# Kernel tuning notes

Hardware: AMD Instinct MI355X
Metric: run time of the kernel (lower is better)

## Reference

```python
import jax, jax.numpy as jnp
import numpy as np

B, L, H, NH, HD, IT = 16, 512, 256, 8, 32, 2
NEG = -9e15


def _ln(x, g, b):
    m = x.mean(-1, keepdims=True)
    v = ((x - m) ** 2).mean(-1, keepdims=True)
    return (x - m) / jnp.sqrt(v + 1e-5) * g + b


def setup_inputs() -> dict:
    key = jax.random.key(0)
    ks = jax.random.split(key, 12)

    def nrm(k, shape, fan_in):
        return jax.random.normal(k, shape, dtype=jnp.float32) / np.float32(np.sqrt(fan_in))

    return {
        "data": jax.random.normal(ks[0], (B, L, H), jnp.float32),
        "gat_WQ_w": nrm(ks[1], (NH, H, H), H),
        "gat_WQ_b": jnp.zeros((NH, H), jnp.float32),
        "gat_a1": nrm(ks[2], (NH, 3 * H), 3 * H),
        "gat_a2": nrm(ks[3], (NH, 3 * H), 3 * H),
        "gat_fc_w": nrm(ks[4], (NH, 3 * H, HD), 3 * H),
        "gat_fc_b": jnp.zeros((NH, HD), jnp.float32),
        "norm_g": jnp.ones((IT, H), jnp.float32),
        "norm_b": jnp.zeros((IT, H), jnp.float32),
        "sq_w": nrm(ks[5], (IT, NH * HD, H), H),
        "sq_b": jnp.zeros((IT, NH * HD), jnp.float32),
        "sk_w": nrm(ks[6], (IT, NH * HD, H), H),
        "sk_b": jnp.zeros((IT, NH * HD), jnp.float32),
        "so_w": nrm(ks[7], (IT, H, NH * HD), NH * HD),
        "so_b": jnp.zeros((IT, H), jnp.float32),
        "fc_w": nrm(ks[8], (NH * HD, H), NH * HD),
        "fc_b": jnp.zeros((H,), jnp.float32),
        "mask": jax.random.randint(ks[9], (B, L), 0, 2, jnp.int32),
        "edge_matrix": jax.random.randint(ks[10], (B, L, L), 0, 2, jnp.int32),
    }


def _gat_head(xn, ax, adj_pos, Wq, bq, a1, a2, Fw, Fb):
    # xn: [B,L,H] normalized nodes; ax: [B,L,2H] interleaved (r_embs, relay)
    h = jnp.concatenate([xn @ Wq.T + bq, ax], axis=-1)  # [B,L,3H]
    # decomposed a^T [h_i ; h_j] = a1.h_i + a2.h_j  (avoids O(N^2*6H) concat)
    ei = h @ a1  # [B,L]
    ej = h @ a2  # [B,L]
    e = jax.nn.leaky_relu(ei[:, :, None] + ej[:, None, :], 0.2)  # [B,L,L]
    att = jax.nn.softmax(jnp.where(adj_pos, e, NEG), axis=2)
    hp = jnp.einsum('bij,bjd->bid', att, h)  # [B,L,3H]
    return jax.nn.elu(hp @ Fw + Fb)  # [B,L,HD]


def _forward(data, gat_WQ_w, gat_WQ_b, gat_a1, gat_a2, gat_fc_w, gat_fc_b,
             norm_g, norm_b, sq_w, sq_b, sk_w, sk_b, so_w, so_b, fc_w, fc_b,
             mask, edge_matrix):
    pad = mask == 0                                   # True at padding positions
    smask = jnp.concatenate([jnp.zeros((B, 1), bool), pad], axis=1)  # [B,L+1]
    adj_pos = edge_matrix > 0
    nodes = data                                      # [B,L,H]
    relay = data.mean(axis=1)                         # [B,H]
    gat = jax.vmap(_gat_head, in_axes=(None, None, None, 0, 0, 0, 0, 0, 0))
    scale = np.float32(1.0 / np.sqrt(HD))

    for i in range(IT):
        xn = _ln(nodes, norm_g[i], norm_b[i])
        # torch views [B,H,2,L] as [B,2H,L]: features interleave (r_embs, relay)
        ax = jnp.stack([data, jnp.broadcast_to(relay[:, None, :], (B, L, H))],
                       axis=-1).reshape(B, L, 2 * H)
        heads = gat(xn, ax, adj_pos, gat_WQ_w, gat_WQ_b, gat_a1, gat_a2,
                    gat_fc_w, gat_fc_b)               # [NH,B,L,HD]
        temp = jnp.transpose(heads, (1, 2, 0, 3)).reshape(B, L, NH * HD)
        nodes = nodes + jax.nn.leaky_relu(temp @ fc_w + fc_b, 0.01)
        # star attention (MSA2); note original uses v = k (WV unused)
        y = jnp.concatenate([relay[:, None, :], nodes], axis=1)   # [B,L+1,H]
        q = (relay @ sq_w[i].T + sq_b[i]).reshape(B, NH, HD)
        k = (y @ sk_w[i].T + sk_b[i]).transpose(0, 2, 1).reshape(B, NH, HD, L + 1)
        v = jnp.swapaxes(k, 2, 3)                                  # [B,NH,L+1,HD]
        pre = jnp.einsum('bnd,bndl->bnl', q, k) * scale
        pre = jnp.where(smask[:, None, :], -jnp.inf, pre)
        al = jax.nn.softmax(pre, axis=2)
        att = jnp.einsum('bnl,bnld->bnd', al, v).reshape(B, NH * HD)
        relay = jax.nn.leaky_relu(att @ so_w[i].T + so_b[i], 0.01)
        nodes = jnp.where(pad[:, :, None], 0.0, nodes)
    return nodes, relay


def reference(data, gat_WQ_w, gat_WQ_b, gat_a1, gat_a2, gat_fc_w, gat_fc_b,
              norm_g, norm_b, sq_w, sq_b, sk_w, sk_b, so_w, so_b, fc_w, fc_b,
              mask, edge_matrix):
    return _forward(data, gat_WQ_w, gat_WQ_b, gat_a1, gat_a2, gat_fc_w, gat_fc_b,
                    norm_g, norm_b, sq_w, sq_b, sk_w, sk_b, so_w, so_b, fc_w, fc_b,
                    mask, edge_matrix)
```

## Files before the change

### kernel.cpp

```cpp
#include <hip/hip_runtime.h>
#include <hip/hip_bf16.h>
#include <math.h>

#define BB 16
#define LL 512
#define HH 256
#define NHEAD 8
#define HDIM 32
#define LP1 513
#define NODES_ELEMS (BB*LL*HH)

typedef __attribute__((ext_vector_type(8))) short bf16x8;
typedef __attribute__((ext_vector_type(4))) float f32x4;

__device__ __forceinline__ unsigned short f2bf(float f) {
  union { float f; unsigned u; } x; x.f = f;
  unsigned r = x.u + 0x7fffu + ((x.u >> 16) & 1u);
  return (unsigned short)(r >> 16);
}
__device__ __forceinline__ float bf2f(unsigned short u) {
  union { unsigned u; float f; } x; x.u = (unsigned)u << 16; return x.f;
}

__global__ __launch_bounds__(256) void mega_prep_kernel(
    const float* __restrict__ data, const int* __restrict__ edge,
    const float* __restrict__ fc_w, const float* __restrict__ fcw,
    const float* __restrict__ sk_w, const float* __restrict__ sq_w,
    const float* __restrict__ so_w, const float* __restrict__ WQw,
    const float* __restrict__ WQb, const float* __restrict__ a1,
    const float* __restrict__ a2,
    unsigned short* __restrict__ datab, unsigned char* __restrict__ ep,
    unsigned short* __restrict__ fcwT, unsigned short* __restrict__ Bcat,
    unsigned short* __restrict__ skwb, float* __restrict__ sqT,
    float* __restrict__ soT, float* __restrict__ rpart,
    float* __restrict__ w1, float* __restrict__ w2,
    float* __restrict__ c1, float* __restrict__ c2,
    float* __restrict__ bqf, float* __restrict__ a1o, float* __restrict__ a2o) {
  __shared__ float smem[64 * 65];
  int blk = blockIdx.x, t = threadIdx.x;
  if (blk < 128) {
    int b = blk >> 3, ch = blk & 7;
    const float* pr = data + ((size_t)b * 512 + ch * 64) * 256 + t;
    unsigned short* db = datab + ((size_t)b * 512 + ch * 64) * 256 + t;
    float s = 0.f;
    for (int l = 0; l < 64; l++) {
      float v = pr[(size_t)l * 256];
      db[(size_t)l * 256] = f2bf(v);
      s += v;
    }
    rpart[(size_t)blk * 256 + t] = s;
  } else if (blk < 2176) {
    int row = (blk - 128) * 4 + (t >> 6);
    int lane = t & 63;
    const int* adj = edge + ((size_t)row << 9);
    unsigned v = 0;
#pragma unroll
    for (int u = 0; u < 8; u++) v |= (adj[lane + 64 * u] > 0 ? 1u : 0u) << u;
    ep[((size_t)row << 6) + lane] = (unsigned char)v;
  } else if (blk < 2432) {
    int idx = (blk - 2176) * 256 + t;
    int d = idx & 31;
    int g = idx >> 5;
    int n = g >> 8, c = g & 255;
    Bcat[((size_t)n * 32 + d) * 512 + 256 + c] =
        f2bf(fcw[((size_t)n * 768 + 256 + 2 * c) * 32 + d]);
  } else if (blk < 2944) {
    int idx = (blk - 2432) * 256 + t;
    skwb[idx] = f2bf(sk_w[idx]);
  } else if (blk < 3024) {
    int q = blk - 2944;
    int mat = q >> 4, tl = q & 15;
    int r0 = (tl >> 2) * 64, c0 = (tl & 3) * 64;
    const float* in;
    if (mat == 0) in = fc_w;
    else if (mat <= 2) in = sq_w + (mat - 1) * 65536;
    else in = so_w + (mat - 3) * 65536;
    int cc = t & 63, rq = t >> 6;
#pragma unroll
    for (int i = 0; i < 16; i++) {
      int r = rq + i * 4;
      smem[r * 65 + cc] = in[(r0 + r) * 256 + c0 + cc];
    }
    __syncthreads();
#pragma unroll
    for (int i = 0; i < 16; i++) {
      int cp = rq + i * 4;
      float v = smem[cc * 65 + cp];
      if (mat == 0) fcwT[(c0 + cp) * 256 + r0 + cc] = f2bf(v);
      else if (mat <= 2) sqT[(mat - 1) * 65536 + (c0 + cp) * 256 + r0 + cc] = v;
      else soT[(mat - 3) * 65536 + (c0 + cp) * 256 + r0 + cc] = v;
    }
  } else if (blk < 3152) {
    int q = blk - 3024;
    int n = q >> 4, kc = q & 15;
    int k = kc * 16 + (t & 15), cseg = t >> 4;
    float s1 = 0.f, s2 = 0.f;
#pragma unroll
    for (int u = 0; u < 16; u++) {
      int c = cseg * 16 + u;
      float wv = WQw[((size_t)(n * 256 + c)) * 256 + k];
      s1 = fmaf(a1[n * 768 + c], wv, s1);
      s2 = fmaf(a2[n * 768 + c], wv, s2);
    }
    smem[cseg * 16 + (t & 15)] = s1;
    smem[256 + cseg * 16 + (t & 15)] = s2;
    __syncthreads();
    if (cseg == 0) {
      float a = 0.f, b2 = 0.f;
#pragma unroll
      for (int u = 0; u < 16; u++) {
        a += smem[u * 16 + (t & 15)];
        b2 += smem[256 + u * 16 + (t & 15)];
      }
      w1[n * 256 + k] = a;
      w2[n * 256 + k] = b2;
    }
  } else if (blk < 3160) {
    int n = blk - 3152;
    int d = t & 31, seg = t >> 5;
    float s = 0.f;
#pragma unroll
    for (int u = 0; u < 32; u++) {
      int c = seg * 32 + u;
      s = fmaf(WQb[n * 256 + c], fcw[((size_t)n * 768 + c) * 32 + d], s);
    }
    smem[seg * 32 + d] = s;
    __syncthreads();
    if (seg == 0) {
      float a = 0.f;
#pragma unroll
      for (int u = 0; u < 8; u++) a += smem[u * 32 + d];
      bqf[n * 32 + d] = a;
    }
  } else if (blk == 3160) {
    int n = t >> 5, sl = t & 31;
    float s1 = 0.f, s2 = 0.f;
#pragma unroll
    for (int u = 0; u < 8; u++) {
      int c = sl * 8 + u;
      float wb = WQb[n * 256 + c];
      s1 = fmaf(a1[n * 768 + c], wb, s1);
      s2 = fmaf(a2[n * 768 + c], wb, s2);
    }
    smem[t] = s1; smem[256 + t] = s2;
    __syncthreads();
    if (sl == 0) {
      float a = 0.f, b2 = 0.f;
      for (int u = 0; u < 32; u++) { a += smem[n * 32 + u]; b2 += smem[256 + n * 32 + u]; }
      c1[n] = a; c2[n] = b2;
    }
  } else {
#pragma unroll
    for (int n = 0; n < 8; n++) {
      a1o[n * 256 + t] = a1[n * 768 + 256 + 2 * t];
      a2o[n * 256 + t] = a2[n * 768 + 256 + 2 * t];
    }
  }
}

__device__ __forceinline__ void rarf_tail(
    int n, int b, int t, const float* rel,
    const float* __restrict__ a1, const float* __restrict__ a2,
    const float* __restrict__ fcw, const float* __restrict__ fcb,
    const float* __restrict__ bqf,
    float* __restrict__ ra1, float* __restrict__ ra2, float* __restrict__ rf,
    float* red1, float* red2, float* pf_s) {
  int lane = t & 63, w = t >> 6;
  float p1 = rel[t] * a1[n * 768 + 257 + 2 * t];
  float p2 = rel[t] * a2[n * 768 + 257 + 2 * t];
#pragma unroll
  for (int o = 32; o; o >>= 1) { p1 += __shfl_xor(p1, o); p2 += __shfl_xor(p2, o); }
  if (lane == 0) { red1[w] = p1; red2[w] = p2; }
  int d = t & 31, seg = t >> 5;
  float pf = 0.f;
  for (int u = 0; u < 32; u++) {
    int k = seg * 32 + u;
    pf = fmaf(rel[k], fcw[((size_t)n * 768 + 257 + 2 * k) * 32 + d], pf);
  }
  pf_s[seg * 33 + d] = pf;
  __syncthreads();
  if (t == 0) {
    ra1[n * 16 + b] = red1[0] + red1[1] + red1[2] + red1[3];
    ra2[n * 16 + b] = red2[0] + red2[1] + red2[2] + red2[3];
  }
  if (t < 32) {
    float s = 0.f;
    for (int gg = 0; gg < 8; gg++) s += pf_s[gg * 33 + t];
    rf[((size_t)n * 16 + b) * 32 + t] = s + fcb[n * 32 + t] + bqf[n * 32 + t];
  }
}

__global__ __launch_bounds__(256) void prep2_kernel(
    const float* __restrict__ WQw, const float* __restrict__ fcw,
    unsigned short* __restrict__ Bcat,
    const float* __restrict__ rpart,
    const unsigned short* __restrict__ skw0, const float* __restrict__ skb0,
    const float* __restrict__ a1, const float* __restrict__ a2,
    const float* __restrict__ fcb, const float* __restrict__ bqf,
    const float* __restrict__ w1, const float* __restrict__ w2,
    const float* __restrict__ a1o, const float* __restrict__ a2o,
    float* __restrict__ relay, unsigned short* __restrict__ ktb,
    float* __restrict__ ra1, float* __restrict__ ra2, float* __restrict__ rf) {
  __shared__ float smem[12288];
  int blk = blockIdx.x, t = threadIdx.x;
  if (blk < 128) {
    float* wq_s = smem;
    float* fw_s = smem + 4096;
    int n = blk >> 4, kt = blk & 15;
#pragma unroll
    for (int i = 0; i < 16; i++) {
      int c = i * 16 + (t >> 4), kk = t & 15;
      wq_s[c * 16 + kk] = WQw[(size_t)n * 65536 + c * 256 + kt * 16 + kk];
    }
#pragma unroll
    for (int i = 0; i < 32; i++) {
      int idx = i * 256 + t;
      fw_s[(idx >> 5) * 32 + (idx & 31)] = fcw[(size_t)n * 24576 + idx];
    }
    __syncthreads();
    int kloc = t >> 4, dp = t & 15;
    float a0 = 0.f, a1v = 0.f;
    for (int c = 0; c < 256; c++) {
      float wv = wq_s[c * 16 + kloc];
      a0 = fmaf(wv, fw_s[c * 32 + dp * 2], a0);
      a1v = fmaf(wv, fw_s[c * 32 + dp * 2 + 1], a1v);
    }
    int k = kt * 16 + kloc;
    Bcat[((size_t)n * 32 + dp * 2) * 512 + k] = f2bf(a0);
    Bcat[((size_t)n * 32 + dp * 2 + 1) * 512 + k] = f2bf(a1v);
  } else if (blk < 256) {
    float* rel = smem;
    float* red1 = smem + 256;
    float* red2 = smem + 264;
    float* pf_s = smem + 272;
    int id = blk - 128;
    int n = id >> 4, b = id & 15;
    float s = 0.f;
#pragma unroll
    for (int ch = 0; ch < 8; ch++) s += rpart[((size_t)(b * 8 + ch)) * 256 + t];
    s *= (1.0f / 512.0f);
    rel[t] = s;
    __syncthreads();
    if (n == 0) {
      relay[b * 256 + t] = s;
      float acc = 0.f;
      for (int k = 0; k < 256; k++) acc = fmaf(rel[k], bf2f(skw0[(size_t)t * 256 + k]), acc);
      ktb[((size_t)b * LP1) * 256 + t] = f2bf(acc + skb0[t]);
    }
    rarf_tail(n, b, t, rel, a1, a2, fcw, fcb, bqf, ra1, ra2, rf, red1, red2, pf_s);
  } else {
    int q = blk - 256;
    int n = q & 7, isEj = q >> 3;
    const float* wsrc = isEj ? w2 : w1;
    const float* asrc = isEj ? a2o : a1o;
#pragma unroll
    for (int h = 0; h < 2; h++) {
      int k = h * 256 + t;
      float v = (k < 256) ? wsrc[n * 256 + k] : asrc[n * 256 + k - 256];
      Bcat[((size_t)(256 + q)) * 512 + k] = f2bf(v);
    }
  }
}

__global__ __launch_bounds__(256) void so_rarf_kernel(
    const float* __restrict__ atts,
    const float* __restrict__ soT_it, const float* __restrict__ sob_it,
    const unsigned short* __restrict__ skw_nx, const float* __restrict__ skb_nx,
    const float* __restrict__ a1, const float* __restrict__ a2,
    const float* __restrict__ fcw, const float* __restrict__ fcb,
    const float* __restrict__ bqf, int do_extras,
    float* __restrict__ relay, unsigned short* __restrict__ ktb,
    float* __restrict__ ra1, float* __restrict__ ra2, float* __restrict__ rf) {
  int n = blockIdx.x >> 4, b = blockIdx.x & 15;
  if (!do_extras && n > 0) return;
  __shared__ float xr[256];
  __shared__ float rel[256];
  __shared__ float red1[4], red2[4];
  __shared__ float pf_s[8 * 33];
  int t = threadIdx.x;
  xr[t] = atts[b * 256 + t];
  __syncthreads();
  float acc = 0.f;
  for (int k = 0; k < 256; k++) acc = fmaf(xr[k], soT_it[(size_t)k * 256 + t], acc);
  float v = acc + sob_it[t];
  v = v > 0.f ? v : 0.01f * v;
  rel[t] = v;
  __syncthreads();
  if (n == 0) relay[b * 256 + t] = v;
  if (!do_extras) return;
  if (n == 0) {
    float a2v = 0.f;
    for (int k = 0; k < 256; k++) a2v = fmaf(rel[k], bf2f(skw_nx[(size_t)t * 256 + k]), a2v);
    ktb[((size_t)b * LP1) * 256 + t] = f2bf(a2v + skb_nx[t]);
  }
  rarf_tail(n, b, t, rel, a1, a2, fcw, fcb, bqf, ra1, ra2, rf, red1, red2, pf_s);
}

__global__ __launch_bounds__(256) void lng_gemm_kernel(
    const float* __restrict__ src,
    const unsigned short* __restrict__ datab,
    const unsigned short* __restrict__ Bcat,
    const float* __restrict__ g, const float* __restrict__ bb,
    const float* __restrict__ c1, const float* __restrict__ c2,
    const float* __restrict__ ra1, const float* __restrict__ ra2,
    unsigned short* __restrict__ GT,
    float* __restrict__ ei, float* __restrict__ ej) {
  __shared__ unsigned short A[32][520];
  int blk = blockIdx.x;
  int b = blk >> 4;
  int i0 = (blk & 15) << 5;
  int t = threadIdx.x;
  int wv = t >> 6, lane = t & 63;
  int lo = lane & 15, quad = lane >> 4;

  float4 g4 = *(const float4*)(g + lane * 4);
  float4 b4 = *(const float4*)(bb + lane * 4);
  float xs[8][4];
  float sum[8], sq[8];
#pragma unroll
  for (int rr = 0; rr < 8; rr++) {
    int grow = b * 512 + i0 + wv * 8 + rr;
    float4 v = *(const float4*)(src + (size_t)grow * 256 + lane * 4);
    xs[rr][0] = v.x; xs[rr][1] = v.y; xs[rr][2] = v.z; xs[rr][3] = v.w;
    sum[rr] = v.x + v.y + v.z + v.w;
    sq[rr] = v.x * v.x + v.y * v.y + v.z * v.z + v.w * v.w;
    ushort4 dv4 = *(const ushort4*)(datab + (size_t)grow * 256 + lane * 4);
    *(ushort4*)&A[wv * 8 + rr][256 + lane * 4] = dv4;
  }
#pragma unroll
  for (int o = 32; o; o >>= 1) {
#pragma unroll
    for (int rr = 0; rr < 8; rr++) {
      sum[rr] += __shfl_xor(sum[rr], o);
      sq[rr] += __shfl_xor(sq[rr], o);
    }
  }
#pragma unroll
  for (int rr = 0; rr < 8; rr++) {
    float mean = sum[rr] * (1.0f / 256.0f);
    float var = sq[rr] * (1.0f / 256.0f) - mean * mean;
    float rstd = rsqrtf(var + 1e-5f);
    ushort4 pk;
    pk.x = f2bf((xs[rr][0] - mean) * rstd * g4.x + b4.x);
    pk.y = f2bf((xs[rr][1] - mean) * rstd * g4.y + b4.y);
    pk.z = f2bf((xs[rr][2] - mean) * rstd * g4.z + b4.z);
    pk.w = f2bf((xs[rr][3] - mean) * rstd * g4.w + b4.w);
    *(ushort4*)&A[wv * 8 + rr][lane * 4] = pk;
  }
  __syncthreads();

  f32x4 acc[2][4] = {};
  f32x4 acce[2] = {};
  for (int k0 = 0; k0 < 512; k0 += 32) {
    bf16x8 af[2];
#pragma unroll
    for (int rt = 0; rt < 2; rt++)
      af[rt] = *(const bf16x8*)&A[rt * 16 + lo][k0 + quad * 8];
#pragma unroll
    for (int j = 0; j < 4; j++) {
      int tile = j * 4 + wv;
      bf16x8 bf_ = *(const bf16x8*)(Bcat + (size_t)(tile * 16 + lo) * 512 + k0 + quad * 8);
#pragma unroll
      for (int rt = 0; rt < 2; rt++)
        acc[rt][j] = __builtin_amdgcn_mfma_f32_16x16x32_bf16(af[rt], bf_, acc[rt][j], 0, 0, 0);
    }
    if (wv == 0) {
      bf16x8 bf_ = *(const bf16x8*)(Bcat + (size_t)(256 + lo) * 512 + k0 + quad * 8);
#pragma unroll
      for (int rt = 0; rt < 2; rt++)
        acce[rt] = __builtin_amdgcn_mfma_f32_16x16x32_bf16(af[rt], bf_, acce[rt], 0, 0, 0);
    }
  }
#pragma unroll
  for (int j = 0; j < 4; j++) {
    int tile = j * 4 + wv;
    int co = tile * 16 + lo;
    int n = co >> 5, d = co & 31;
#pragma unroll
    for (int rt = 0; rt < 2; rt++) {
      int jj = i0 + rt * 16 + quad * 4;
      ushort4 pk;
      pk.x = f2bf(acc[rt][j][0]);
      pk.y = f2bf(acc[rt][j][1]);
      pk.z = f2bf(acc[rt][j][2]);
      pk.w = f2bf(acc[rt][j][3]);
      *(ushort4*)&GT[(((size_t)(n * 16 + b) * 32 + d) << 9) + jj] = pk;
    }
  }
  if (wv == 0) {
    int n = lo & 7, isEj = lo >> 3;
    float cst = isEj ? (c2[n] + ra2[n * 16 + b]) : (c1[n] + ra1[n * 16 + b]);
    float* outp = isEj ? ej : ei;
#pragma unroll
    for (int rt = 0; rt < 2; rt++) {
#pragma unroll
      for (int r = 0; r < 4; r++) {
        int row = i0 + rt * 16 + quad * 4 + r;
        outp[n * 8192 + b * 512 + row] = acce[rt][r] + cst;
      }
    }
  }
}

__global__ __launch_bounds__(256) void gat_agg_kernel(
    const unsigned short* __restrict__ GT,
    const float* __restrict__ ei, const float* __restrict__ ej,
    const unsigned char* __restrict__ ep,
    const float* __restrict__ rf,
    unsigned short* __restrict__ tempb) {
  __shared__ unsigned short W[32][512];
  __shared__ float denom_s[32];
  int blk = blockIdx.x;
  int sib = blk >> 7;
  int g = blk & 127;
  int n = g >> 4;
  int b = g & 15;
  int i0 = sib << 5;
  int t = threadIdx.x;
  int wv = t >> 6, lane = t & 63;
  int lo = lane & 15, quad = lane >> 4;

  const float* ejrow = ej + n * 8192 + b * 512;
  float ejv[8];
#pragma unroll
  for (int u = 0; u < 8; u++) ejv[u] = ejrow[lane + 64 * u];
  float mm = ejv[0];
#pragma unroll
  for (int u = 1; u < 8; u++) mm = fmaxf(mm, ejv[u]);
#pragma unroll
  for (int o = 32; o; o >>= 1) mm = fmaxf(mm, __shfl_xor(mm, o));

  for (int rr = 0; rr < 8; rr++) {
    int row = wv * 8 + rr;
    float eiv = ei[n * 8192 + b * 512 + i0 + row];
    float M = eiv + mm;
    M = M > 0.f ? M : 0.2f * M;
    unsigned pb = ep[(((size_t)(b * 512 + i0 + row)) << 6) + lane];
    int rx = (row & 7) << 3;
#pragma unroll
    for (int u = 0; u < 8; u++) {
      float e = eiv + ejv[u];
      e = e > 0.f ? e : 0.2f * e;
      float w = ((pb >> u) & 1) ? __expf(e - M) : 0.f;
      int col = lane + 64 * u;
      W[row][((col >> 3 << 3) ^ rx) + (col & 7)] = f2bf(w);
    }
  }
  __syncthreads();

  int rt = wv >> 1, dh = wv & 1;
  int arow = rt * 16 + lo;
  int rx = arow & 7;
  const unsigned short* gtb = GT + (((size_t)(n * 16 + b) * 32) << 9);
  bf16x8 bones;
  {
    short ov = (lo == 0) ? (short)0x3F80 : (short)0;
#pragma unroll
    for (int j = 0; j < 8; j++) bones[j] = ov;
  }
  f32x4 acc = {}, accd = {};
  for (int k0 = 0; k0 < 512; k0 += 32) {
    int chunk = (k0 >> 3) + quad;
    bf16x8 a0 = *(const bf16x8*)&W[arow][(chunk ^ rx) << 3];
    bf16x8 bf_ = *(const bf16x8*)(gtb + (((size_t)(dh * 16 + lo)) << 9) + k0 + quad * 8);
    acc = __builtin_amdgcn_mfma_f32_16x16x32_bf16(a0, bf_, acc, 0, 0, 0);
    if (dh == 0)
      accd = __builtin_amdgcn_mfma_f32_16x16x32_bf16(a0, bones, accd, 0, 0, 0);
  }
  if (dh == 0 && lo == 0) {
#pragma unroll
    for (int r = 0; r < 4; r++) denom_s[rt * 16 + quad * 4 + r] = accd[r];
  }
  __syncthreads();
  int d = dh * 16 + lo;
  float base = rf[((size_t)n * 16 + b) * 32 + d];
#pragma unroll
  for (int r = 0; r < 4; r++) {
    int row = rt * 16 + quad * 4 + r;
    float inv = 1.0f / fmaxf(denom_s[row], 1e-35f);
    float v = acc[r] * inv + base;
    v = v > 0.f ? v : expm1f(v);
    tempb[((size_t)(b * 512 + i0 + row)) * 256 + n * 32 + d] = f2bf(v);
  }
}

__global__ __launch_bounds__(256) void fc_kt_kernel(
    const unsigned short* __restrict__ tempb,
    const unsigned short* __restrict__ fcwT,
    const float* __restrict__ fc_b,
    const unsigned short* __restrict__ skw_it,
    const float* __restrict__ skb_it,
    const int* __restrict__ mask,
    const float* __restrict__ resid,
    float* __restrict__ nodes,
    unsigned short* __restrict__ ktb) {
  __shared__ unsigned short tmp[32][264];
  int blk = blockIdx.x;
  int b = blk >> 4;
  int i0 = (blk & 15) << 5;
  int t = threadIdx.x;
  int wv = t >> 6, lane = t & 63;
  int lo = lane & 15, quad = lane >> 4;
  int ch = wv >> 1, rt2 = wv & 1;

  const unsigned short* arow_p = tempb + ((size_t)(b * 512 + i0 + rt2 * 16 + lo)) * 256 + quad * 8;
  f32x4 facc[8] = {};
  for (int k0 = 0; k0 < 256; k0 += 32) {
    bf16x8 a0 = *(const bf16x8*)(arow_p + k0);
#pragma unroll
    for (int ct = 0; ct < 8; ct++) {
      int co = ch * 128 + ct * 16 + lo;
      bf16x8 bf_ = *(const bf16x8*)(fcwT + (size_t)co * 256 + k0 + quad * 8);
      facc[ct] = __builtin_amdgcn_mfma_f32_16x16x32_bf16(a0, bf_, facc[ct], 0, 0, 0);
    }
  }
#pragma unroll
  for (int ct = 0; ct < 8; ct++) {
    int co = ch * 128 + ct * 16 + lo;
    float bv = fc_b[co];
#pragma unroll
    for (int r = 0; r < 4; r++) {
      int row = rt2 * 16 + quad * 4 + r;
      int grow = b * 512 + i0 + row;
      float v = facc[ct][r] + bv;
      v = v > 0.f ? v : 0.01f * v;
      v = (mask[grow] != 0) ? resid[(size_t)grow * 256 + co] + v : 0.f;
      nodes[(size_t)grow * 256 + co] = v;
      tmp[row][co] = f2bf(v);
    }
  }
  __syncthreads();

  f32x4 kacc[8] = {};
  for (int k0 = 0; k0 < 256; k0 += 32) {
    bf16x8 a0 = *(const bf16x8*)&tmp[rt2 * 16 + lo][k0 + quad * 8];
#pragma unroll
    for (int ct = 0; ct < 8; ct++) {
      int co = ch * 128 + ct * 16 + lo;
      bf16x8 bf_ = *(const bf16x8*)(skw_it + (size_t)co * 256 + k0 + quad * 8);
      kacc[ct] = __builtin_amdgcn_mfma_f32_16x16x32_bf16(a0, bf_, kacc[ct], 0, 0, 0);
    }
  }
#pragma unroll
  for (int ct = 0; ct < 8; ct++) {
    int co = ch * 128 + ct * 16 + lo;
    float bv = skb_it[co];
#pragma unroll
    for (int r = 0; r < 4; r++) {
      int row = rt2 * 16 + quad * 4 + r;
      int yrow = b * LP1 + 1 + i0 + row;
      ktb[(size_t)yrow * 256 + co] = f2bf(kacc[ct][r] + bv);
    }
  }
}

__global__ __launch_bounds__(256) void star_attn_kernel(const float* __restrict__ relay,
                                                        const float* __restrict__ sqT_it,
                                                        const float* __restrict__ sqb_it,
                                                        const unsigned short* __restrict__ ktb,
                                                        const int* __restrict__ mask,
                                                        float* __restrict__ attstar) {
  int n = blockIdx.x >> 4, b = blockIdx.x & 15;
  int t = threadIdx.x;
  int lane = t & 63, w = t >> 6;
  __shared__ float relb[256];
  __shared__ float qv[32];
  __shared__ float pre[LP1];
  __shared__ float red[4];
  __shared__ float par[8][33];
  relb[t] = relay[b * 256 + t];
  __syncthreads();
  {
    int d = t & 31, g = t >> 5;
    float qp = 0.f;
    for (int k = 0; k < 32; k++)
      qp = fmaf(relb[g * 32 + k], sqT_it[(size_t)(g * 32 + k) * 256 + n * 32 + d], qp);
    par[g][d] = qp;
  }
  __syncthreads();
  if (t < 32) {
    float q = 0.f;
#pragma unroll
    for (int gg = 0; gg < 8; gg++) q += par[gg][t];
    qv[t] = q + sqb_it[n * 32 + t];
  }
  __syncthreads();
  const float scale = 0.17677669529663687f;
  for (int l = t; l < LP1; l += 256) {
    bool masked = (l > 0) && (mask[b * LL + l - 1] == 0);
    float p;
    if (masked) p = -3.4e38f;
    else {
      p = 0.f;
      const unsigned short* krow = ktb + ((size_t)b * LP1 + l) * 256 + n * 32;
#pragma unroll
      for (int d = 0; d < 32; d++) p = fmaf(qv[d], bf2f(krow[d]), p);
      p *= scale;
    }
    pre[l] = p;
  }
  __syncthreads();
  float m = -3.4e38f;
  for (int l = t; l < LP1; l += 256) m = fmaxf(m, pre[l]);
#pragma unroll
  for (int o = 32; o; o >>= 1) m = fmaxf(m, __shfl_xor(m, o));
  if (lane == 0) red[w] = m;
  __syncthreads();
  m = fmaxf(fmaxf(red[0], red[1]), fmaxf(red[2], red[3]));
  __syncthreads();
  float s = 0.f;
  for (int l = t; l < LP1; l += 256) {
    float wv = __expf(pre[l] - m);
    pre[l] = wv;
    s += wv;
  }
#pragma unroll
  for (int o = 32; o; o >>= 1) s += __shfl_xor(s, o);
  if (lane == 0) red[w] = s;
  __syncthreads();
  float denom = red[0] + red[1] + red[2] + red[3];
  int d = t & 31, g = t >> 5;
  float acc = 0.f;
  for (int l = g; l < LP1; l += 8)
    acc = fmaf(pre[l], bf2f(ktb[((size_t)b * LP1 + l) * 256 + n * 32 + d]), acc);
  par[g][d] = acc;
  __syncthreads();
  if (t < 32) {
    float a = 0.f;
    for (int gg = 0; gg < 8; gg++) a += par[gg][t];
    attstar[b * 256 + n * 32 + t] = a / denom;
  }
}

extern "C" void kernel_launch(void* const* d_in, const int* in_sizes, int n_in,
                              void* d_out, int out_size, void* d_ws, size_t ws_size,
                              hipStream_t stream) {
  const float* data  = (const float*)d_in[0];
  const float* WQw   = (const float*)d_in[1];
  const float* WQb   = (const float*)d_in[2];
  const float* a1    = (const float*)d_in[3];
  const float* a2    = (const float*)d_in[4];
  const float* fcw_g = (const float*)d_in[5];
  const float* fcb_g = (const float*)d_in[6];
  const float* ng    = (const float*)d_in[7];
  const float* nb    = (const float*)d_in[8];
  const float* sq_w  = (const float*)d_in[9];
  const float* sq_b  = (const float*)d_in[10];
  const float* sk_w  = (const float*)d_in[11];
  const float* sk_b  = (const float*)d_in[12];
  const float* so_w  = (const float*)d_in[13];
  const float* so_b  = (const float*)d_in[14];
  const float* fc_w  = (const float*)d_in[15];
  const float* fc_b  = (const float*)d_in[16];
  const int*   mask  = (const int*)d_in[17];
  const int*   edge  = (const int*)d_in[18];

  float* nodes = (float*)d_out;
  float* relay = nodes + NODES_ELEMS;

  char* p = (char*)d_ws;
  auto alloc = [&](size_t bytes) -> char* {
    char* r = p; p += (bytes + 255) & ~(size_t)255; return r;
  };
  unsigned short* datab= (unsigned short*)alloc((size_t)8192 * 256 * 2);
  unsigned short* GT   = (unsigned short*)alloc((size_t)8 * 16 * 32 * 512 * 2);
  unsigned short* tmpb = (unsigned short*)alloc((size_t)8192 * 256 * 2);
  unsigned short* ktb  = (unsigned short*)alloc((size_t)8208 * 256 * 2);
  unsigned char* ep    = (unsigned char*)alloc((size_t)8192 * 64);
  float* ei            = (float*)alloc(65536 * 4);
  float* ej            = (float*)alloc(65536 * 4);
  float* ra1           = (float*)alloc(128 * 4);
  float* ra2           = (float*)alloc(128 * 4);
  float* rf            = (float*)alloc(4096 * 4);
  float* bqf           = (float*)alloc(256 * 4);
  float* w1            = (float*)alloc(2048 * 4);
  float* w2            = (float*)alloc(2048 * 4);
  float* c1            = (float*)alloc(8 * 4);
  float* c2            = (float*)alloc(8 * 4);
  float* a1o           = (float*)alloc(2048 * 4);
  float* a2o           = (float*)alloc(2048 * 4);
  float* rpart         = (float*)alloc(128 * 256 * 4);
  unsigned short* Bcat = (unsigned short*)alloc((size_t)288 * 512 * 2);
  unsigned short* fcwT = (unsigned short*)alloc((size_t)65536 * 2);
  unsigned short* skwb = (unsigned short*)alloc((size_t)131072 * 2);
  float* sqT           = (float*)alloc((size_t)131072 * 4);
  float* soT           = (float*)alloc((size_t)131072 * 4);
  float* atts          = (float*)alloc(4096 * 4);

  mega_prep_kernel<<<3162, 256, 0, stream>>>(data, edge, fc_w, fcw_g, sk_w, sq_w,
                                             so_w, WQw, WQb, a1, a2,
                                             datab, ep, fcwT, Bcat, skwb, sqT, soT,
                                             rpart, w1, w2, c1, c2, bqf, a1o, a2o);
  prep2_kernel<<<272, 256, 0, stream>>>(WQw, fcw_g, Bcat, rpart, skwb, sk_b,
                                        a1, a2, fcb_g, bqf, w1, w2, a1o, a2o,
                                        relay, ktb, ra1, ra2, rf);

  for (int it = 0; it < 2; it++) {
    const float* src = (it == 0) ? data : nodes;
    lng_gemm_kernel<<<256, 256, 0, stream>>>(src, datab, Bcat,
                                             ng + it * 256, nb + it * 256,
                                             c1, c2, ra1, ra2, GT, ei, ej);
    gat_agg_kernel<<<NHEAD * BB * 16, 256, 0, stream>>>(GT, ei, ej, ep, rf, tmpb);
    fc_kt_kernel<<<256, 256, 0, stream>>>(tmpb, fcwT, fc_b,
                                          skwb + it * 65536, sk_b + it * 256,
                                          mask, src, nodes, ktb);
    star_attn_kernel<<<BB * NHEAD, 256, 0, stream>>>(relay, sqT + it * 65536,
                                                     sq_b + it * 256, ktb, mask, atts);
    so_rarf_kernel<<<128, 256, 0, stream>>>(atts, soT + it * 65536, so_b + it * 256,
                                            skwb + 65536, sk_b + 256,
                                            a1, a2, fcw_g, fcb_g, bqf,
                                            (it == 0) ? 1 : 0,
                                            relay, ktb, ra1, ra2, rf);
  }
}
```

Baseline: 328.3 us.

## Vectorize adjacency packing, ej loads, W stores and key reads; reorder block mapping

The adjacency bitmask packing now reads 8 contiguous ints per lane instead of a 64-strided pattern, which changes the bit-to-column mapping. The attention kernel loads ej as two float4s and writes each row's 8 weights as a single 16-byte swizzled LDS store, consistent with the new mapping. The star-attention key dot product reads bf16x8 vectors instead of scalar shorts. The lng_gemm and fc_kt kernels swap the block index decomposition so consecutive blocks walk batches first. The aim is fewer memory transactions and bank conflicts, at the cost of touching several kernels that must agree on the new column mapping.

Measured after the change: 322.1 us, median of 2. Within noise of the previous version (-1.9%).

```diff
diff --git a/kernel.cpp b/kernel.cpp
--- a/kernel.cpp
+++ b/kernel.cpp
@@ -52,10 +52,10 @@
   } else if (blk < 2176) {
     int row = (blk - 128) * 4 + (t >> 6);
     int lane = t & 63;
-    const int* adj = edge + ((size_t)row << 9);
+    const int* adj = edge + ((size_t)row << 9) + lane * 8;
     unsigned v = 0;
 #pragma unroll
-    for (int u = 0; u < 8; u++) v |= (adj[lane + 64 * u] > 0 ? 1u : 0u) << u;
+    for (int u = 0; u < 8; u++) v |= (adj[u] > 0 ? 1u : 0u) << u;
     ep[((size_t)row << 6) + lane] = (unsigned char)v;
   } else if (blk < 2432) {
     int idx = (blk - 2176) * 256 + t;
@@ -307,8 +307,8 @@
     float* __restrict__ ei, float* __restrict__ ej) {
   __shared__ unsigned short A[32][520];
   int blk = blockIdx.x;
-  int b = blk >> 4;
-  int i0 = (blk & 15) << 5;
+  int b = blk & 15;
+  int i0 = (blk >> 4) << 5;
   int t = threadIdx.x;
   int wv = t >> 6, lane = t & 63;
   int lo = lane & 15, quad = lane >> 4;
@@ -422,8 +422,12 @@
 
   const float* ejrow = ej + n * 8192 + b * 512;
   float ejv[8];
-#pragma unroll
-  for (int u = 0; u < 8; u++) ejv[u] = ejrow[lane + 64 * u];
+  {
+    float4 e0 = *(const float4*)(ejrow + lane * 8);
+    float4 e1 = *(const float4*)(ejrow + lane * 8 + 4);
+    ejv[0] = e0.x; ejv[1] = e0.y; ejv[2] = e0.z; ejv[3] = e0.w;
+    ejv[4] = e1.x; ejv[5] = e1.y; ejv[6] = e1.z; ejv[7] = e1.w;
+  }
   float mm = ejv[0];
 #pragma unroll
   for (int u = 1; u < 8; u++) mm = fmaxf(mm, ejv[u]);
@@ -435,16 +439,16 @@
     float eiv = ei[n * 8192 + b * 512 + i0 + row];
     float M = eiv + mm;
     M = M > 0.f ? M : 0.2f * M;
-    unsigned pb = ep[(((size_t)(b * 512 + i0 + row)) << 6) + lane];
-    int rx = (row & 7) << 3;
+    unsigned pbv = ep[(((size_t)(b * 512 + i0 + row)) << 6) + lane];
+    bf16x8 wpack;
 #pragma unroll
     for (int u = 0; u < 8; u++) {
       float e = eiv + ejv[u];
       e = e > 0.f ? e : 0.2f * e;
-      float w = ((pb >> u) & 1) ? __expf(e - M) : 0.f;
-      int col = lane + 64 * u;
-      W[row][((col >> 3 << 3) ^ rx) + (col & 7)] = f2bf(w);
-    }
+      float w = ((pbv >> u) & 1) ? __expf(e - M) : 0.f;
+      wpack[u] = (short)f2bf(w);
+    }
+    *(bf16x8*)&W[row][(lane ^ (row & 7)) << 3] = wpack;
   }
   __syncthreads();
 
@@ -496,8 +500,8 @@
     unsigned short* __restrict__ ktb) {
   __shared__ unsigned short tmp[32][264];
   int blk = blockIdx.x;
-  int b = blk >> 4;
-  int i0 = (blk & 15) << 5;
+  int b = blk & 15;
+  int i0 = (blk >> 4) << 5;
   int t = threadIdx.x;
   int wv = t >> 6, lane = t & 63;
   int lo = lane & 15, quad = lane >> 4;
@@ -592,9 +596,14 @@
     if (masked) p = -3.4e38f;
     else {
       p = 0.f;
-      const unsigned short* krow = ktb + ((size_t)b * LP1 + l) * 256 + n * 32;
-#pragma unroll
-      for (int d = 0; d < 32; d++) p = fmaf(qv[d], bf2f(krow[d]), p);
+      const bf16x8* krow8 = (const bf16x8*)(ktb + ((size_t)b * LP1 + l) * 256 + n * 32);
+#pragma unroll
+      for (int dd = 0; dd < 4; dd++) {
+        bf16x8 kv = krow8[dd];
+#pragma unroll
+        for (int j = 0; j < 8; j++)
+          p = fmaf(qv[dd * 8 + j], bf2f((unsigned short)kv[j]), p);
+      }
       p *= scale;
     }
     pre[l] = p;
```
